# Performance work log

Measured on AMD Instinct MI355X. Metric: run time of the kernel, lower is better.

## Reference

```python
import jax, jax.numpy as jnp
import numpy as np

B_TRUE, S, HEADS, DIM_HEAD, DIM, N = 2, 2, 8, 64, 512, 1024
BS = B_TRUE * S            # effective batch = (b s)
DIM_INNER = HEADS * DIM_HEAD
ALL_HEADS = S * HEADS
EPS = 1e-5


def setup_inputs() -> dict:
    key = jax.random.key(0)
    ks = jax.random.split(key, 8)
    inv = 0.02
    x = jax.random.normal(ks[0], (BS, N, DIM), dtype=jnp.float32)
    mask = jax.random.randint(ks[1], (BS, N), 0, 2).astype(bool)
    gamma = jnp.ones((DIM,), dtype=jnp.float32)
    w_qkv = jax.random.normal(ks[2], (3 * DIM_INNER, DIM), dtype=jnp.float32) * inv
    w_gates = jax.random.normal(ks[3], (HEADS, DIM), dtype=jnp.float32) * inv
    b_gates = jnp.zeros((HEADS,), dtype=jnp.float32)
    w_pre = jax.random.normal(ks[4], (ALL_HEADS, ALL_HEADS), dtype=jnp.float32) * 0.25
    w_post = jax.random.normal(ks[5], (ALL_HEADS, ALL_HEADS), dtype=jnp.float32) * 0.25
    w_out = jax.random.normal(ks[6], (DIM, DIM_INNER), dtype=jnp.float32) * inv
    return {"x": x, "mask": mask, "gamma": gamma, "w_qkv": w_qkv,
            "w_gates": w_gates, "b_gates": b_gates, "w_pre": w_pre,
            "w_post": w_post, "w_out": w_out}


def _rmsnorm(x, gamma):
    # einn.Norm('b... [d]', mean=False, bias=False): RMSNorm over last dim
    var = jnp.mean(jnp.square(x), axis=-1, keepdims=True)
    return x * jax.lax.rsqrt(var + EPS) * gamma


def reference(x, mask, gamma, w_qkv, w_gates, b_gates, w_pre, w_post, w_out):
    bs, n, dim = x.shape
    b = bs // S
    x = _rmsnorm(x, gamma)

    # QKV: 'b n (qkv h d) -> qkv b h n d'
    qkv = jnp.einsum('bnd,ed->bne', x, w_qkv)
    qkv = qkv.reshape(bs, n, 3, HEADS, DIM_HEAD).transpose(2, 0, 3, 1, 4)
    q, k, v = qkv[0], qkv[1], qkv[2]
    q = q * (DIM_HEAD ** 0.5)  # NOTE: source MULTIPLIES by sqrt(dim_head)

    sim = jnp.einsum('bhid,bhjd->bhij', q, k)  # [bs, h, n, n]
    mask_value = -jnp.finfo(sim.dtype).max

    # pre talking-heads: 1x1 conv across (s h) channels
    sim = sim.reshape(b, ALL_HEADS, n, n)
    sim = jnp.einsum('oi,binm->bonm', w_pre, sim).reshape(bs, HEADS, n, n)

    # padding mask over keys j
    sim = jnp.where(mask[:, None, None, :], sim, mask_value)

    # causal mask
    causal = jnp.triu(jnp.ones((n, n), dtype=bool), 1)
    sim = jnp.where(causal, mask_value, sim)

    attn = jax.nn.softmax(sim, axis=-1)
    post_softmax_attn = attn

    # post talking-heads
    attn = attn.reshape(b, ALL_HEADS, n, n)
    attn = jnp.einsum('oi,binm->bonm', w_post, attn).reshape(bs, HEADS, n, n)

    out = jnp.einsum('bhij,bhjd->bhid', attn, v)  # [bs, h, n, d]

    # sigmoid gates from normed x: 'b n h -> b h n 1'
    gates = jax.nn.sigmoid(jnp.einsum('bnd,hd->bnh', x, w_gates) + b_gates)
    out = out * gates.transpose(0, 2, 1)[..., None]

    # 'b h n d -> b n (h d)' then Linear(dim_inner, dim, bias=False)
    out = out.transpose(0, 2, 1, 3).reshape(bs, n, DIM_INNER)
    out = jnp.einsum('bne,de->bnd', out, w_out)
    return (out, post_softmax_attn)
```

## Files before the change

kernel.cpp:

```cpp
#include <hip/hip_runtime.h>
#include <cfloat>
#include <math.h>

#define B2   2
#define BS4  4
#define NH   8
#define DH   64
#define DIM  512
#define NSEQ 1024
#define AH   16

typedef __attribute__((ext_vector_type(8))) short short8;
typedef __attribute__((ext_vector_type(4))) float floatx4;
typedef __attribute__((ext_vector_type(2))) float float2v;

__device__ inline unsigned short f2bf(float x) {
    unsigned int u = __float_as_uint(x);
    unsigned int r = (u + 0x7fffu + ((u >> 16) & 1u)) >> 16;
    return (unsigned short)r;
}
__device__ inline float bf2f(unsigned short h) {
    return __uint_as_float(((unsigned int)h) << 16);
}
__device__ inline void split2(float x, unsigned short& h, unsigned short& l) {
    h = f2bf(x);
    l = f2bf(x - bf2f(h));
}

__device__ inline float2v pk_fma(float2v a, float2v b, float2v c) {
#if __has_builtin(__builtin_elementwise_fma)
    return __builtin_elementwise_fma(a, b, c);
#else
    float2v r;
    r[0] = fmaf(a[0], b[0], c[0]);
    r[1] = fmaf(a[1], b[1], c[1]);
    return r;
#endif
}

template<int MT, int NT_, bool SPLIT>
__device__ inline void mfma_nt_core(
    const unsigned short* __restrict__ Ah, const unsigned short* __restrict__ Al,
    const unsigned short* __restrict__ Bh, const unsigned short* __restrict__ Bl,
    int K, int lda, int ldb, int arow, int bcol, floatx4 acc[MT][NT_])
{
    int lane = threadIdx.x & 63;
    int lr = lane & 15, lq = lane >> 4;
    for (int k0 = 0; k0 < K; k0 += 32) {
        short8 ah[MT], al[MT], bh[NT_], bl[NT_];
        #pragma unroll
        for (int mi = 0; mi < MT; ++mi) {
            size_t off = (size_t)(arow + mi * 16 + lr) * lda + k0 + lq * 8;
            ah[mi] = *(const short8*)(Ah + off);
            if (SPLIT) al[mi] = *(const short8*)(Al + off);
        }
        #pragma unroll
        for (int ni = 0; ni < NT_; ++ni) {
            size_t off = (size_t)(bcol + ni * 16 + lr) * ldb + k0 + lq * 8;
            bh[ni] = *(const short8*)(Bh + off);
            if (SPLIT) bl[ni] = *(const short8*)(Bl + off);
        }
        #pragma unroll
        for (int mi = 0; mi < MT; ++mi)
            #pragma unroll
            for (int ni = 0; ni < NT_; ++ni) {
                acc[mi][ni] = __builtin_amdgcn_mfma_f32_16x16x32_bf16(ah[mi], bh[ni], acc[mi][ni], 0, 0, 0);
                if (SPLIT) {
                    acc[mi][ni] = __builtin_amdgcn_mfma_f32_16x16x32_bf16(ah[mi], bl[ni], acc[mi][ni], 0, 0, 0);
                    acc[mi][ni] = __builtin_amdgcn_mfma_f32_16x16x32_bf16(al[mi], bh[ni], acc[mi][ni], 0, 0, 0);
                }
            }
    }
}

__global__ __launch_bounds__(256) void k_rmsnorm_gates(
    const float* __restrict__ x, const float* __restrict__ gamma,
    const float* __restrict__ wg, const float* __restrict__ bg,
    unsigned short* __restrict__ xn_h, unsigned short* __restrict__ xn_l,
    float* __restrict__ gates)
{
    int r = blockIdx.x;
    int tid = threadIdx.x;
    const float* xr = x + (size_t)r * DIM;
    float v0 = xr[tid];
    float v1 = xr[tid + 256];
    float ss = v0 * v0 + v1 * v1;
    #pragma unroll
    for (int off = 32; off > 0; off >>= 1) ss += __shfl_down(ss, off, 64);
    __shared__ float sc[4];
    __shared__ float scw[NH][4];
    if ((tid & 63) == 0) sc[tid >> 6] = ss;
    __syncthreads();
    float tot = sc[0] + sc[1] + sc[2] + sc[3];
    float rs = rsqrtf(tot * (1.0f / DIM) + 1e-5f);
    float n0 = v0 * rs * gamma[tid];
    float n1 = v1 * rs * gamma[tid + 256];
    unsigned short hh, ll;
    split2(n0, hh, ll);
    xn_h[(size_t)r * DIM + tid] = hh; xn_l[(size_t)r * DIM + tid] = ll;
    split2(n1, hh, ll);
    xn_h[(size_t)r * DIM + tid + 256] = hh; xn_l[(size_t)r * DIM + tid + 256] = ll;
    #pragma unroll
    for (int h = 0; h < NH; ++h) {
        float p = n0 * wg[h * DIM + tid] + n1 * wg[h * DIM + tid + 256];
        #pragma unroll
        for (int off = 32; off > 0; off >>= 1) p += __shfl_down(p, off, 64);
        if ((tid & 63) == 0) scw[h][tid >> 6] = p;
    }
    __syncthreads();
    if (tid < NH) {
        float g = scw[tid][0] + scw[tid][1] + scw[tid][2] + scw[tid][3] + bg[tid];
        gates[(size_t)r * NH + tid] = 1.0f / (1.0f + __expf(-g));
    }
}

#define NQKV (3 * DIM * NH * DH)
#define NOUT (DIM * NH * DH)
__global__ __launch_bounds__(256) void k_cvt(
    const float* __restrict__ wqkv, const float* __restrict__ wout,
    unsigned short* __restrict__ wq_h, unsigned short* __restrict__ wq_l,
    unsigned short* __restrict__ wout_b)
{
    for (int i = blockIdx.x * 256 + threadIdx.x; i < NQKV + NOUT; i += gridDim.x * 256) {
        if (i < NQKV) {
            unsigned short hh, ll;
            split2(wqkv[i], hh, ll);
            wq_h[i] = hh; wq_l[i] = ll;
        } else {
            wout_b[i - NQKV] = f2bf(wout[i - NQKV]);
        }
    }
}

__global__ __launch_bounds__(256) void k_qkv_mfma(
    const unsigned short* __restrict__ xn_h, const unsigned short* __restrict__ xn_l,
    const unsigned short* __restrict__ wq_h, const unsigned short* __restrict__ wq_l,
    unsigned short* __restrict__ q_h, unsigned short* __restrict__ q_l,
    unsigned short* __restrict__ k_h, unsigned short* __restrict__ k_l,
    unsigned short* __restrict__ vT_b)
{
    __shared__ unsigned short vs[64][132];
    int w = threadIdx.x >> 6;
    int bx = blockIdx.x;
    int am = blockIdx.y * 128 + (w & 1) * 64;
    int bn = bx * 64 + (w >> 1) * 32;
    floatx4 acc[4][2];
    #pragma unroll
    for (int mi = 0; mi < 4; ++mi)
        #pragma unroll
        for (int ni = 0; ni < 2; ++ni) acc[mi][ni] = (floatx4){0.f, 0.f, 0.f, 0.f};
    mfma_nt_core<4, 2, true>(xn_h, xn_l, wq_h, wq_l, DIM, DIM, DIM, am, bn, acc);
    int tid = threadIdx.x;
    int lane = tid & 63, lr = lane & 15, lq = lane >> 4;

    if (bx < 16) {
        const bool isq = (bx < 8);
        unsigned short* dh = isq ? q_h : k_h;
        unsigned short* dl = isq ? q_l : k_l;
        const float scale = isq ? 8.0f : 1.0f;
        #pragma unroll
        for (int mi = 0; mi < 4; ++mi)
            #pragma unroll
            for (int ni = 0; ni < 2; ++ni)
                #pragma unroll
                for (int r = 0; r < 4; ++r) {
                    int row = am + mi * 16 + lq * 4 + r;
                    int col = bn + ni * 16 + lr;
                    int bs = row >> 10, npos = row & 1023;
                    int h = (col >> 6) & 7, d = col & 63;
                    size_t idx = (((size_t)(bs * 8 + h)) * NSEQ + npos) * DH + d;
                    unsigned short hh, ll;
                    split2(acc[mi][ni][r] * scale, hh, ll);
                    dh[idx] = hh; dl[idx] = ll;
                }
    } else {
        const int h = bx - 16;
        const int bs = (blockIdx.y * 128) >> 10;
        const int bh = bs * 8 + h;
        const int npos_base = (blockIdx.y * 128) & 1023;
        #pragma unroll
        for (int mi = 0; mi < 4; ++mi)
            #pragma unroll
            for (int ni = 0; ni < 2; ++ni)
                #pragma unroll
                for (int r = 0; r < 4; ++r) {
                    int nl = (w & 1) * 64 + mi * 16 + lq * 4 + r;
                    int dl2 = (w >> 1) * 32 + ni * 16 + lr;
                    vs[dl2][nl] = f2bf(acc[mi][ni][r]);
                }
        __syncthreads();
        int d = tid >> 2;
        int sub = tid & 3;
        unsigned short* dst = vT_b + ((size_t)bh * DH + d) * NSEQ + npos_base;
        #pragma unroll
        for (int it = 0; it < 4; ++it) {
            int nl = sub * 8 + it * 32;
            *(ulonglong2*)(dst + nl) = *(ulonglong2*)&vs[d][nl];
        }
    }
}

__global__ __launch_bounds__(256) void k_qk_mfma(
    const unsigned short* __restrict__ q_h, const unsigned short* __restrict__ q_l,
    const unsigned short* __restrict__ k_h, const unsigned short* __restrict__ k_l,
    float* __restrict__ sim_ws)
{
    __shared__ float cs[128][68];
    int bh = blockIdx.z;
    int b_true = bh >> 4;
    int c = ((bh >> 3) & 1) * 8 + (bh & 7);
    int w = threadIdx.x >> 6;
    int am = blockIdx.y * 128 + (w & 1) * 64;
    int bn = blockIdx.x * 64 + (w >> 1) * 32;
    const unsigned short* Ah = q_h + (size_t)bh * NSEQ * DH;
    const unsigned short* Al = q_l + (size_t)bh * NSEQ * DH;
    const unsigned short* Bh = k_h + (size_t)bh * NSEQ * DH;
    const unsigned short* Bl = k_l + (size_t)bh * NSEQ * DH;
    floatx4 acc[4][2];
    #pragma unroll
    for (int mi = 0; mi < 4; ++mi)
        #pragma unroll
        for (int ni = 0; ni < 2; ++ni) acc[mi][ni] = (floatx4){0.f, 0.f, 0.f, 0.f};
    mfma_nt_core<4, 2, true>(Ah, Al, Bh, Bl, DH, DH, DH, am, bn, acc);

    int tid = threadIdx.x;
    int lane = tid & 63, lr = lane & 15, lq = lane >> 4;
    #pragma unroll
    for (int mi = 0; mi < 4; ++mi)
        #pragma unroll
        for (int ni = 0; ni < 2; ++ni)
            #pragma unroll
            for (int r = 0; r < 4; ++r) {
                int lrow = (w & 1) * 64 + mi * 16 + lq * 4 + r;
                int lcol = (w >> 1) * 32 + ni * 16 + lr;
                cs[lrow][lcol] = acc[mi][ni][r];
            }
    __syncthreads();
    int trow = tid >> 4;
    int tcol = (tid & 15) * 4;
    int am0 = blockIdx.y * 128;
    int bn0 = blockIdx.x * 64;
    #pragma unroll
    for (int it = 0; it < 8; ++it) {
        int row = it * 16 + trow;
        float4 v4 = *(float4*)&cs[row][tcol];
        size_t gaddr = ((size_t)(b_true * NSEQ + am0 + row) * 16 + c) * NSEQ + bn0 + tcol;
        *(float4*)(sim_ws + gaddr) = v4;
    }
}

__global__ __launch_bounds__(256) void k_talk(
    float* __restrict__ sim_ws, const int* __restrict__ mask,
    const float* __restrict__ wpre, const float* __restrict__ wpost,
    float* __restrict__ probs_out)
{
    const int i = blockIdx.x;
    const int b = blockIdx.y;
    const int tid = threadIdx.x;
    const int wid = tid >> 6, lane = tid & 63;
    const int j0 = tid << 2;
    const size_t cstride = (size_t)NSEQ * NSEQ;
    float* simrow = sim_ws + (size_t)(b * NSEQ + i) * (16 * NSEQ);

    const int4 mi0 = *(const int4*)(mask + (size_t)(b * 2 + 0) * NSEQ + j0);
    const int4 mi1 = *(const int4*)(mask + (size_t)(b * 2 + 1) * NSEQ + j0);
    bool mb[2][4];
    mb[0][0] = (mi0.x != 0) && (j0 + 0 <= i);
    mb[0][1] = (mi0.y != 0) && (j0 + 1 <= i);
    mb[0][2] = (mi0.z != 0) && (j0 + 2 <= i);
    mb[0][3] = (mi0.w != 0) && (j0 + 3 <= i);
    mb[1][0] = (mi1.x != 0) && (j0 + 0 <= i);
    mb[1][1] = (mi1.y != 0) && (j0 + 1 <= i);
    mb[1][2] = (mi1.z != 0) && (j0 + 2 <= i);
    mb[1][3] = (mi1.w != 0) && (j0 + 3 <= i);

    float2v val[16][2];
    #pragma unroll
    for (int o = 0; o < 16; ++o) {
        val[o][0] = (float2v){0.f, 0.f};
        val[o][1] = (float2v){0.f, 0.f};
    }
    #pragma unroll
    for (int c = 0; c < 16; ++c) {
        float4 r = *(const float4*)(simrow + c * NSEQ + j0);
        float2v r01 = (float2v){r.x, r.y};
        float2v r23 = (float2v){r.z, r.w};
        #pragma unroll
        for (int o = 0; o < 16; ++o) {
            float w = wpre[o * 16 + c];
            float2v wv = (float2v){w, w};
            val[o][0] = pk_fma(wv, r01, val[o][0]);
            val[o][1] = pk_fma(wv, r23, val[o][1]);
        }
    }
    #pragma unroll
    for (int o = 0; o < 16; ++o) {
        const int s = o >> 3;
        if (!mb[s][0]) val[o][0][0] = -FLT_MAX;
        if (!mb[s][1]) val[o][0][1] = -FLT_MAX;
        if (!mb[s][2]) val[o][1][0] = -FLT_MAX;
        if (!mb[s][3]) val[o][1][1] = -FLT_MAX;
    }

    __shared__ float red[16][4];
    __shared__ float finmx[16];
    __shared__ float fininv[16];

    #pragma unroll
    for (int o = 0; o < 16; ++o) {
        float m = fmaxf(fmaxf(val[o][0][0], val[o][0][1]), fmaxf(val[o][1][0], val[o][1][1]));
        #pragma unroll
        for (int off = 32; off > 0; off >>= 1) m = fmaxf(m, __shfl_xor(m, off, 64));
        if (lane == 0) red[o][wid] = m;
    }
    __syncthreads();
    if (tid < 16)
        finmx[tid] = fmaxf(fmaxf(red[tid][0], red[tid][1]), fmaxf(red[tid][2], red[tid][3]));
    __syncthreads();

    #pragma unroll
    for (int o = 0; o < 16; ++o) {
        float mx = finmx[o];
        float e0 = __expf(val[o][0][0] - mx);
        float e1 = __expf(val[o][0][1] - mx);
        float e2 = __expf(val[o][1][0] - mx);
        float e3 = __expf(val[o][1][1] - mx);
        val[o][0][0] = e0; val[o][0][1] = e1;
        val[o][1][0] = e2; val[o][1][1] = e3;
        float s = (e0 + e1) + (e2 + e3);
        #pragma unroll
        for (int off = 32; off > 0; off >>= 1) s += __shfl_xor(s, off, 64);
        if (lane == 0) red[o][wid] = s;
    }
    __syncthreads();
    if (tid < 16)
        fininv[tid] = 1.0f / (red[tid][0] + red[tid][1] + red[tid][2] + red[tid][3]);
    __syncthreads();

    #pragma unroll
    for (int o = 0; o < 16; ++o) {
        float inv = fininv[o];
        float2v invv = (float2v){inv, inv};
        val[o][0] *= invv;
        val[o][1] *= invv;
        floatx4 st = {val[o][0][0], val[o][0][1], val[o][1][0], val[o][1][1]};
        __builtin_nontemporal_store(st,
            (floatx4*)(probs_out + (size_t)(b * 16 + o) * cstride + (size_t)i * NSEQ + j0));
    }

    unsigned short* a2row = (unsigned short*)simrow;
    #pragma unroll
    for (int o = 0; o < 16; ++o) {
        float2v a01 = (float2v){0.f, 0.f};
        float2v a23 = (float2v){0.f, 0.f};
        #pragma unroll
        for (int c = 0; c < 16; ++c) {
            float w = wpost[o * 16 + c];
            float2v wv = (float2v){w, w};
            a01 = pk_fma(wv, val[c][0], a01);
            a23 = pk_fma(wv, val[c][1], a23);
        }
        unsigned long long pk = (unsigned long long)f2bf(a01[0])
                              | ((unsigned long long)f2bf(a01[1]) << 16)
                              | ((unsigned long long)f2bf(a23[0]) << 32)
                              | ((unsigned long long)f2bf(a23[1]) << 48);
        *(unsigned long long*)(a2row + o * NSEQ + j0) = pk;
    }
}

__global__ __launch_bounds__(256) void k_av_mfma(
    const unsigned short* __restrict__ attn2_il, const unsigned short* __restrict__ vT_b,
    const float* __restrict__ gates, unsigned short* __restrict__ gated_b)
{
    int bh = blockIdx.y;
    int bs = bh >> 3, h = bh & 7;
    int b_true = bh >> 4;
    int c = ((bh >> 3) & 1) * 8 + (bh & 7);
    int w = threadIdx.x >> 6;
    int am = blockIdx.x * 64 + (w & 1) * 32;
    int bn = (w >> 1) * 32;
    const unsigned short* Ah = attn2_il + (size_t)b_true * NSEQ * 32768 + (size_t)c * NSEQ;
    const unsigned short* Bh = vT_b + (size_t)bh * DH * NSEQ;
    floatx4 acc[2][2];
    #pragma unroll
    for (int mi = 0; mi < 2; ++mi)
        #pragma unroll
        for (int ni = 0; ni < 2; ++ni) acc[mi][ni] = (floatx4){0.f, 0.f, 0.f, 0.f};
    mfma_nt_core<2, 2, false>(Ah, nullptr, Bh, nullptr, NSEQ, 32768, NSEQ, am, bn, acc);
    int lane = threadIdx.x & 63, lr = lane & 15, lq = lane >> 4;
    #pragma unroll
    for (int mi = 0; mi < 2; ++mi)
        #pragma unroll
        for (int ni = 0; ni < 2; ++ni)
            #pragma unroll
            for (int r = 0; r < 4; ++r) {
                int i = am + mi * 16 + lq * 4 + r;
                int d = bn + ni * 16 + lr;
                float g = gates[((size_t)bs * NSEQ + i) * NH + h];
                gated_b[((size_t)bs * NSEQ + i) * DIM + h * DH + d] = f2bf(acc[mi][ni][r] * g);
            }
}

__global__ __launch_bounds__(256) void k_out_mfma(
    const unsigned short* __restrict__ gated_b, const unsigned short* __restrict__ wout_b,
    float* __restrict__ out)
{
    int w = threadIdx.x >> 6;
    int am = blockIdx.y * 64 + (w & 1) * 32;
    int bn = blockIdx.x * 64 + (w >> 1) * 32;
    floatx4 acc[2][2];
    #pragma unroll
    for (int mi = 0; mi < 2; ++mi)
        #pragma unroll
        for (int ni = 0; ni < 2; ++ni) acc[mi][ni] = (floatx4){0.f, 0.f, 0.f, 0.f};
    mfma_nt_core<2, 2, false>(gated_b, nullptr, wout_b, nullptr, DIM, DIM, DIM, am, bn, acc);
    int lane = threadIdx.x & 63, lr = lane & 15, lq = lane >> 4;
    #pragma unroll
    for (int mi = 0; mi < 2; ++mi)
        #pragma unroll
        for (int ni = 0; ni < 2; ++ni)
            #pragma unroll
            for (int r = 0; r < 4; ++r) {
                int row = am + mi * 16 + lq * 4 + r;
                int col = bn + ni * 16 + lr;
                out[(size_t)row * DIM + col] = acc[mi][ni][r];
            }
}

extern "C" void kernel_launch(void* const* d_in, const int* in_sizes, int n_in,
                              void* d_out, int out_size, void* d_ws, size_t ws_size,
                              hipStream_t stream)
{
    (void)in_sizes; (void)n_in; (void)out_size; (void)ws_size;

    const float* x     = (const float*)d_in[0];
    const int*   mask  = (const int*)  d_in[1];
    const float* gamma = (const float*)d_in[2];
    const float* wqkv  = (const float*)d_in[3];
    const float* wg    = (const float*)d_in[4];
    const float* bg    = (const float*)d_in[5];
    const float* wpre  = (const float*)d_in[6];
    const float* wpost = (const float*)d_in[7];
    const float* wout  = (const float*)d_in[8];

    float* out       = (float*)d_out;
    float* probs_out = out + (size_t)BS4 * NSEQ * DIM;

    char* ws = (char*)d_ws;
    unsigned short* xn_h    = (unsigned short*)(ws);
    unsigned short* xn_l    = (unsigned short*)(ws + 4194304);
    unsigned short* wq_h    = (unsigned short*)(ws + 8388608);
    unsigned short* wq_l    = (unsigned short*)(ws + 9961472);
    unsigned short* wout_b  = (unsigned short*)(ws + 11534336);
    float*          gates   = (float*)         (ws + 12058624);
    unsigned short* q_h     = (unsigned short*)(ws + 12189696);
    unsigned short* q_l     = (unsigned short*)(ws + 16384000);
    unsigned short* k_h     = (unsigned short*)(ws + 20578304);
    unsigned short* k_l     = (unsigned short*)(ws + 24772608);
    unsigned short* vT_b    = (unsigned short*)(ws + 28966912);
    unsigned short* gated_b = (unsigned short*)(ws + 33161216);
    float*          sim_ws  = (float*)         (ws + 37355520);

    k_rmsnorm_gates<<<dim3(BS4 * NSEQ), dim3(256), 0, stream>>>(x, gamma, wg, bg, xn_h, xn_l, gates);
    k_cvt<<<dim3(1024), dim3(256), 0, stream>>>(wqkv, wout, wq_h, wq_l, wout_b);
    k_qkv_mfma<<<dim3(24, 32), dim3(256), 0, stream>>>(xn_h, xn_l, wq_h, wq_l, q_h, q_l, k_h, k_l, vT_b);
    k_qk_mfma<<<dim3(16, 8, 32), dim3(256), 0, stream>>>(q_h, q_l, k_h, k_l, sim_ws);
    k_talk<<<dim3(NSEQ, B2), dim3(256), 0, stream>>>(sim_ws, mask, wpre, wpost, probs_out);
    k_av_mfma<<<dim3(16, 32), dim3(256), 0, stream>>>((unsigned short*)sim_ws, vT_b, gates, gated_b);
    k_out_mfma<<<dim3(8, 64), dim3(256), 0, stream>>>(gated_b, wout_b, out);
}
```

Measured before the change: 401.9 us.

## Use single-wave 64x64 MFMA tiles and skip causally masked QK tiles

```diff
diff --git a/kernel.cpp b/kernel.cpp
--- a/kernel.cpp
+++ b/kernel.cpp
@@ -132,24 +132,23 @@
     }
 }
 
-__global__ __launch_bounds__(256) void k_qkv_mfma(
+__global__ __launch_bounds__(64) void k_qkv_mfma(
     const unsigned short* __restrict__ xn_h, const unsigned short* __restrict__ xn_l,
     const unsigned short* __restrict__ wq_h, const unsigned short* __restrict__ wq_l,
     unsigned short* __restrict__ q_h, unsigned short* __restrict__ q_l,
     unsigned short* __restrict__ k_h, unsigned short* __restrict__ k_l,
     unsigned short* __restrict__ vT_b)
 {
-    __shared__ unsigned short vs[64][132];
-    int w = threadIdx.x >> 6;
+    __shared__ unsigned short vs[64][68];
     int bx = blockIdx.x;
-    int am = blockIdx.y * 128 + (w & 1) * 64;
-    int bn = bx * 64 + (w >> 1) * 32;
-    floatx4 acc[4][2];
-    #pragma unroll
-    for (int mi = 0; mi < 4; ++mi)
-        #pragma unroll
-        for (int ni = 0; ni < 2; ++ni) acc[mi][ni] = (floatx4){0.f, 0.f, 0.f, 0.f};
-    mfma_nt_core<4, 2, true>(xn_h, xn_l, wq_h, wq_l, DIM, DIM, DIM, am, bn, acc);
+    int am = blockIdx.y * 64;
+    int bn = bx * 64;
+    floatx4 acc[4][4];
+    #pragma unroll
+    for (int mi = 0; mi < 4; ++mi)
+        #pragma unroll
+        for (int ni = 0; ni < 4; ++ni) acc[mi][ni] = (floatx4){0.f, 0.f, 0.f, 0.f};
+    mfma_nt_core<4, 4, true>(xn_h, xn_l, wq_h, wq_l, DIM, DIM, DIM, am, bn, acc);
     int tid = threadIdx.x;
     int lane = tid & 63, lr = lane & 15, lq = lane >> 4;
 
@@ -161,7 +160,7 @@
         #pragma unroll
         for (int mi = 0; mi < 4; ++mi)
             #pragma unroll
-            for (int ni = 0; ni < 2; ++ni)
+            for (int ni = 0; ni < 4; ++ni)
                 #pragma unroll
                 for (int r = 0; r < 4; ++r) {
                     int row = am + mi * 16 + lq * 4 + r;
@@ -175,74 +174,71 @@
                 }
     } else {
         const int h = bx - 16;
-        const int bs = (blockIdx.y * 128) >> 10;
+        const int bs = (blockIdx.y * 64) >> 10;
         const int bh = bs * 8 + h;
-        const int npos_base = (blockIdx.y * 128) & 1023;
+        const int npos_base = (blockIdx.y * 64) & 1023;
         #pragma unroll
         for (int mi = 0; mi < 4; ++mi)
             #pragma unroll
-            for (int ni = 0; ni < 2; ++ni)
+            for (int ni = 0; ni < 4; ++ni)
                 #pragma unroll
                 for (int r = 0; r < 4; ++r) {
-                    int nl = (w & 1) * 64 + mi * 16 + lq * 4 + r;
-                    int dl2 = (w >> 1) * 32 + ni * 16 + lr;
+                    int nl  = mi * 16 + lq * 4 + r;
+                    int dl2 = ni * 16 + lr;
                     vs[dl2][nl] = f2bf(acc[mi][ni][r]);
                 }
         __syncthreads();
-        int d = tid >> 2;
-        int sub = tid & 3;
-        unsigned short* dst = vT_b + ((size_t)bh * DH + d) * NSEQ + npos_base;
-        #pragma unroll
-        for (int it = 0; it < 4; ++it) {
-            int nl = sub * 8 + it * 32;
-            *(ulonglong2*)(dst + nl) = *(ulonglong2*)&vs[d][nl];
-        }
-    }
-}
-
-__global__ __launch_bounds__(256) void k_qk_mfma(
+        #pragma unroll
+        for (int it = 0; it < 8; ++it) {
+            int d = it * 8 + (tid >> 3);
+            int c8 = (tid & 7) * 8;
+            unsigned short* dst = vT_b + ((size_t)bh * DH + d) * NSEQ + npos_base + c8;
+            *(ulonglong2*)dst = *(ulonglong2*)&vs[d][c8];
+        }
+    }
+}
+
+__global__ __launch_bounds__(64) void k_qk_mfma(
     const unsigned short* __restrict__ q_h, const unsigned short* __restrict__ q_l,
     const unsigned short* __restrict__ k_h, const unsigned short* __restrict__ k_l,
     float* __restrict__ sim_ws)
 {
-    __shared__ float cs[128][68];
+    __shared__ float cs[64][68];
+    int am0 = blockIdx.y * 64;
+    int bn0 = blockIdx.x * 64;
+    if (bn0 > am0 + 63) return;
     int bh = blockIdx.z;
     int b_true = bh >> 4;
     int c = ((bh >> 3) & 1) * 8 + (bh & 7);
-    int w = threadIdx.x >> 6;
-    int am = blockIdx.y * 128 + (w & 1) * 64;
-    int bn = blockIdx.x * 64 + (w >> 1) * 32;
     const unsigned short* Ah = q_h + (size_t)bh * NSEQ * DH;
     const unsigned short* Al = q_l + (size_t)bh * NSEQ * DH;
     const unsigned short* Bh = k_h + (size_t)bh * NSEQ * DH;
     const unsigned short* Bl = k_l + (size_t)bh * NSEQ * DH;
-    floatx4 acc[4][2];
-    #pragma unroll
-    for (int mi = 0; mi < 4; ++mi)
-        #pragma unroll
-        for (int ni = 0; ni < 2; ++ni) acc[mi][ni] = (floatx4){0.f, 0.f, 0.f, 0.f};
-    mfma_nt_core<4, 2, true>(Ah, Al, Bh, Bl, DH, DH, DH, am, bn, acc);
+    floatx4 acc[4][4];
+    #pragma unroll
+    for (int mi = 0; mi < 4; ++mi)
+        #pragma unroll
+        for (int ni = 0; ni < 4; ++ni) acc[mi][ni] = (floatx4){0.f, 0.f, 0.f, 0.f};
+    mfma_nt_core<4, 4, true>(Ah, Al, Bh, Bl, DH, DH, DH, am0, bn0, acc);
 
     int tid = threadIdx.x;
     int lane = tid & 63, lr = lane & 15, lq = lane >> 4;
     #pragma unroll
     for (int mi = 0; mi < 4; ++mi)
         #pragma unroll
-        for (int ni = 0; ni < 2; ++ni)
+        for (int ni = 0; ni < 4; ++ni)
             #pragma unroll
             for (int r = 0; r < 4; ++r) {
-                int lrow = (w & 1) * 64 + mi * 16 + lq * 4 + r;
-                int lcol = (w >> 1) * 32 + ni * 16 + lr;
+                int lrow = mi * 16 + lq * 4 + r;
+                int lcol = ni * 16 + lr;
                 cs[lrow][lcol] = acc[mi][ni][r];
             }
     __syncthreads();
     int trow = tid >> 4;
     int tcol = (tid & 15) * 4;
-    int am0 = blockIdx.y * 128;
-    int bn0 = blockIdx.x * 64;
-    #pragma unroll
-    for (int it = 0; it < 8; ++it) {
-        int row = it * 16 + trow;
+    #pragma unroll
+    for (int it = 0; it < 16; ++it) {
+        int row = it * 4 + trow;
         float4 v4 = *(float4*)&cs[row][tcol];
         size_t gaddr = ((size_t)(b_true * NSEQ + am0 + row) * 16 + c) * NSEQ + bn0 + tcol;
         *(float4*)(sim_ws + gaddr) = v4;
@@ -368,7 +364,7 @@
     }
 }
 
-__global__ __launch_bounds__(256) void k_av_mfma(
+__global__ __launch_bounds__(64) void k_av_mfma(
     const unsigned short* __restrict__ attn2_il, const unsigned short* __restrict__ vT_b,
     const float* __restrict__ gates, unsigned short* __restrict__ gated_b)
 {
@@ -376,49 +372,46 @@
     int bs = bh >> 3, h = bh & 7;
     int b_true = bh >> 4;
     int c = ((bh >> 3) & 1) * 8 + (bh & 7);
-    int w = threadIdx.x >> 6;
-    int am = blockIdx.x * 64 + (w & 1) * 32;
-    int bn = (w >> 1) * 32;
+    int am = blockIdx.x * 64;
     const unsigned short* Ah = attn2_il + (size_t)b_true * NSEQ * 32768 + (size_t)c * NSEQ;
     const unsigned short* Bh = vT_b + (size_t)bh * DH * NSEQ;
-    floatx4 acc[2][2];
-    #pragma unroll
-    for (int mi = 0; mi < 2; ++mi)
-        #pragma unroll
-        for (int ni = 0; ni < 2; ++ni) acc[mi][ni] = (floatx4){0.f, 0.f, 0.f, 0.f};
-    mfma_nt_core<2, 2, false>(Ah, nullptr, Bh, nullptr, NSEQ, 32768, NSEQ, am, bn, acc);
+    floatx4 acc[4][4];
+    #pragma unroll
+    for (int mi = 0; mi < 4; ++mi)
+        #pragma unroll
+        for (int ni = 0; ni < 4; ++ni) acc[mi][ni] = (floatx4){0.f, 0.f, 0.f, 0.f};
+    mfma_nt_core<4, 4, false>(Ah, nullptr, Bh, nullptr, NSEQ, 32768, NSEQ, am, 0, acc);
     int lane = threadIdx.x & 63, lr = lane & 15, lq = lane >> 4;
     #pragma unroll
-    for (int mi = 0; mi < 2; ++mi)
-        #pragma unroll
-        for (int ni = 0; ni < 2; ++ni)
+    for (int mi = 0; mi < 4; ++mi)
+        #pragma unroll
+        for (int ni = 0; ni < 4; ++ni)
             #pragma unroll
             for (int r = 0; r < 4; ++r) {
                 int i = am + mi * 16 + lq * 4 + r;
-                int d = bn + ni * 16 + lr;
+                int d = ni * 16 + lr;
                 float g = gates[((size_t)bs * NSEQ + i) * NH + h];
                 gated_b[((size_t)bs * NSEQ + i) * DIM + h * DH + d] = f2bf(acc[mi][ni][r] * g);
             }
 }
 
-__global__ __launch_bounds__(256) void k_out_mfma(
+__global__ __launch_bounds__(64) void k_out_mfma(
     const unsigned short* __restrict__ gated_b, const unsigned short* __restrict__ wout_b,
     float* __restrict__ out)
 {
-    int w = threadIdx.x >> 6;
-    int am = blockIdx.y * 64 + (w & 1) * 32;
-    int bn = blockIdx.x * 64 + (w >> 1) * 32;
-    floatx4 acc[2][2];
-    #pragma unroll
-    for (int mi = 0; mi < 2; ++mi)
-        #pragma unroll
-        for (int ni = 0; ni < 2; ++ni) acc[mi][ni] = (floatx4){0.f, 0.f, 0.f, 0.f};
-    mfma_nt_core<2, 2, false>(gated_b, nullptr, wout_b, nullptr, DIM, DIM, DIM, am, bn, acc);
+    int am = blockIdx.y * 64;
+    int bn = blockIdx.x * 64;
+    floatx4 acc[4][4];
+    #pragma unroll
+    for (int mi = 0; mi < 4; ++mi)
+        #pragma unroll
+        for (int ni = 0; ni < 4; ++ni) acc[mi][ni] = (floatx4){0.f, 0.f, 0.f, 0.f};
+    mfma_nt_core<4, 4, false>(gated_b, nullptr, wout_b, nullptr, DIM, DIM, DIM, am, bn, acc);
     int lane = threadIdx.x & 63, lr = lane & 15, lq = lane >> 4;
     #pragma unroll
-    for (int mi = 0; mi < 2; ++mi)
-        #pragma unroll
-        for (int ni = 0; ni < 2; ++ni)
+    for (int mi = 0; mi < 4; ++mi)
+        #pragma unroll
+        for (int ni = 0; ni < 4; ++ni)
             #pragma unroll
             for (int r = 0; r < 4; ++r) {
                 int row = am + mi * 16 + lq * 4 + r;
@@ -463,9 +456,9 @@
 
     k_rmsnorm_gates<<<dim3(BS4 * NSEQ), dim3(256), 0, stream>>>(x, gamma, wg, bg, xn_h, xn_l, gates);
     k_cvt<<<dim3(1024), dim3(256), 0, stream>>>(wqkv, wout, wq_h, wq_l, wout_b);
-    k_qkv_mfma<<<dim3(24, 32), dim3(256), 0, stream>>>(xn_h, xn_l, wq_h, wq_l, q_h, q_l, k_h, k_l, vT_b);
-    k_qk_mfma<<<dim3(16, 8, 32), dim3(256), 0, stream>>>(q_h, q_l, k_h, k_l, sim_ws);
+    k_qkv_mfma<<<dim3(24, 64), dim3(64), 0, stream>>>(xn_h, xn_l, wq_h, wq_l, q_h, q_l, k_h, k_l, vT_b);
+    k_qk_mfma<<<dim3(16, 16, 32), dim3(64), 0, stream>>>(q_h, q_l, k_h, k_l, sim_ws);
     k_talk<<<dim3(NSEQ, B2), dim3(256), 0, stream>>>(sim_ws, mask, wpre, wpost, probs_out);
-    k_av_mfma<<<dim3(16, 32), dim3(256), 0, stream>>>((unsigned short*)sim_ws, vT_b, gates, gated_b);
-    k_out_mfma<<<dim3(8, 64), dim3(256), 0, stream>>>(gated_b, wout_b, out);
-}
+    k_av_mfma<<<dim3(16, 32), dim3(64), 0, stream>>>((unsigned short*)sim_ws, vT_b, gates, gated_b);
+    k_out_mfma<<<dim3(8, 64), dim3(64), 0, stream>>>(gated_b, wout_b, out);
+}
```

New measurement: 373.4 us. 7.1% less time.
